# Kernel tuning notes

Measured on AMD Instinct MI355X. Metric: run time of the kernel, lower is better.

## Reference

```python
import jax, jax.numpy as jnp
import numpy as np

B, C, D, H, W = 4, 64, 16, 32, 32
K = 1024  # num_embeddings


def setup_inputs() -> dict:
    key = jax.random.key(0)
    k1, k2 = jax.random.split(key)
    z_e = jax.random.normal(k1, (B, C, D, H, W), dtype=jnp.float32)
    embedding = jax.random.normal(k2, (K, C), dtype=jnp.float32)
    return {"z_e": z_e, "embedding": embedding}


def reference(z_e, embedding):
    Bb, Cc, Dd, Hh, Ww = z_e.shape
    # (B, D, H, W, C) -> (N, C)
    flat = jnp.transpose(z_e, (0, 2, 3, 4, 1)).reshape(-1, Cc)
    # squared-euclidean distances to codebook: [N, K]
    distances = (
        jnp.sum(flat * flat, axis=1, keepdims=True)
        - 2.0 * flat @ embedding.T
        + jnp.sum(embedding * embedding, axis=1)
    )
    encoding_indices = jnp.argmin(distances, axis=1)  # [N]
    # one_hot @ embedding == gather (same math, efficient form)
    quantized_flat = embedding[encoding_indices]  # [N, C]
    quantized = jnp.transpose(
        quantized_flat.reshape(Bb, Dd, Hh, Ww, Cc), (0, 4, 1, 2, 3)
    )
    commitment_loss = jnp.mean((jax.lax.stop_gradient(quantized) - z_e) ** 2)
    codebook_loss = jnp.mean((quantized - jax.lax.stop_gradient(z_e)) ** 2)
    # straight-through estimator
    quantized_st = z_e + jax.lax.stop_gradient(quantized - z_e)
    indices = encoding_indices.reshape(Bb, Dd, Hh, Ww)
    return quantized_st, codebook_loss, commitment_loss, indices
```

## Files before the change

kernel.cpp:

```cpp
#include <hip/hip_runtime.h>

#define NPOS    65536
#define CDIM    64
#define KCODES  1024
#define SPATIAL 16384
#define QELEMS  4194304

#define PB      128
#define KT      128
#define NTILE   8

#define LOSS_IDX 1024

__device__ __forceinline__ int sig(int q)  { return (q >> 1) | ((q & 1) << 4); }
__device__ __forceinline__ int xcol(int p) { return 4 * sig(p >> 2) + (p & 3); }

__global__ void k_norms(const float* __restrict__ emb, float* __restrict__ wsf) {
    const int k = blockIdx.x * 256 + threadIdx.x;
    if (k == 0) wsf[LOSS_IDX] = 0.0f;
    const float4* e4 = (const float4*)(emb + (size_t)k * CDIM);
    float s = 0.0f;
#pragma unroll
    for (int c = 0; c < CDIM / 4; ++c) {
        float4 e = e4[c];
        s += e.x * e.x + e.y * e.y + e.z * e.z + e.w * e.w;
    }
    wsf[k] = s;
}

#define FMA_ROW(i, xs) \
    acc[i][0] = fmaf(xs, ea.x, acc[i][0]); acc[i][1] = fmaf(xs, ea.y, acc[i][1]); \
    acc[i][2] = fmaf(xs, ea.z, acc[i][2]); acc[i][3] = fmaf(xs, ea.w, acc[i][3]); \
    acc[i][4] = fmaf(xs, eb.x, acc[i][4]); acc[i][5] = fmaf(xs, eb.y, acc[i][5]); \
    acc[i][6] = fmaf(xs, eb.z, acc[i][6]); acc[i][7] = fmaf(xs, eb.w, acc[i][7]);

__global__ void k_fused(const float* __restrict__ z_e,
                        const float* __restrict__ emb,
                        float* __restrict__ out,
                        float* __restrict__ wsf) {
    __shared__ float XT[CDIM][PB];
    __shared__ float ET[CDIM][KT];
    __shared__ float NRM[KCODES];
    __shared__ unsigned long long bestp[PB];
    __shared__ int bi[PB];

    const int t    = threadIdx.x;
    const int tx   = t & 15;
    const int ty   = t >> 4;
    const int n0   = blockIdx.x * PB;
    const int b    = n0 >> 14;
    const int dhw0 = n0 & (SPATIAL - 1);
    const float* zb = z_e + (size_t)b * (CDIM * SPATIAL) + dhw0;

#pragma unroll
    for (int i = 0; i < 32; ++i) {
        const int idx = i * 256 + t;
        const int c = idx >> 7, p = idx & 127;
        XT[c][xcol(p)] = zb[(size_t)c * SPATIAL + p];
    }
    *(float4*)&NRM[4 * t] = *(const float4*)(wsf + 4 * t);

    const int crow  = t & 127;
    const int cpart = (t >> 7) << 5;
    const int ecol  = xcol(crow);
    float4 g0, g1, g2, g3, g4, g5, g6, g7;
    {
        const float* es = emb + (size_t)crow * CDIM + cpart;
        g0 = *(const float4*)(es +  0); g1 = *(const float4*)(es +  4);
        g2 = *(const float4*)(es +  8); g3 = *(const float4*)(es + 12);
        g4 = *(const float4*)(es + 16); g5 = *(const float4*)(es + 20);
        g6 = *(const float4*)(es + 24); g7 = *(const float4*)(es + 28);
    }

    unsigned long long best8[8];
#pragma unroll
    for (int i = 0; i < 8; ++i) best8[i] = ~0ull;

#pragma unroll 1
    for (int tile = 0; tile < NTILE; ++tile) {
        __syncthreads();
        ET[cpart +  0][ecol] = g0.x; ET[cpart +  1][ecol] = g0.y;
        ET[cpart +  2][ecol] = g0.z; ET[cpart +  3][ecol] = g0.w;
        ET[cpart +  4][ecol] = g1.x; ET[cpart +  5][ecol] = g1.y;
        ET[cpart +  6][ecol] = g1.z; ET[cpart +  7][ecol] = g1.w;
        ET[cpart +  8][ecol] = g2.x; ET[cpart +  9][ecol] = g2.y;
        ET[cpart + 10][ecol] = g2.z; ET[cpart + 11][ecol] = g2.w;
        ET[cpart + 12][ecol] = g3.x; ET[cpart + 13][ecol] = g3.y;
        ET[cpart + 14][ecol] = g3.z; ET[cpart + 15][ecol] = g3.w;
        ET[cpart + 16][ecol] = g4.x; ET[cpart + 17][ecol] = g4.y;
        ET[cpart + 18][ecol] = g4.z; ET[cpart + 19][ecol] = g4.w;
        ET[cpart + 20][ecol] = g5.x; ET[cpart + 21][ecol] = g5.y;
        ET[cpart + 22][ecol] = g5.z; ET[cpart + 23][ecol] = g5.w;
        ET[cpart + 24][ecol] = g6.x; ET[cpart + 25][ecol] = g6.y;
        ET[cpart + 26][ecol] = g6.z; ET[cpart + 27][ecol] = g6.w;
        ET[cpart + 28][ecol] = g7.x; ET[cpart + 29][ecol] = g7.y;
        ET[cpart + 30][ecol] = g7.z; ET[cpart + 31][ecol] = g7.w;
        if (tile + 1 < NTILE) {
            const float* es = emb + (size_t)((tile + 1) * KT + crow) * CDIM + cpart;
            g0 = *(const float4*)(es +  0); g1 = *(const float4*)(es +  4);
            g2 = *(const float4*)(es +  8); g3 = *(const float4*)(es + 12);
            g4 = *(const float4*)(es + 16); g5 = *(const float4*)(es + 20);
            g6 = *(const float4*)(es + 24); g7 = *(const float4*)(es + 28);
        }
        __syncthreads();

        float acc[8][8];
#pragma unroll
        for (int i = 0; i < 8; ++i)
#pragma unroll
            for (int j = 0; j < 8; ++j) acc[i][j] = 0.0f;

        for (int g = 0; g < 16; ++g) {
#pragma unroll
            for (int cj = 0; cj < 4; ++cj) {
                const int ch = 4 * g + cj;
                const float4 ea = *(const float4*)&ET[ch][4 * tx];
                const float4 eb = *(const float4*)&ET[ch][4 * tx + 64];
                const float4 xa = *(const float4*)&XT[ch][4 * ty];
                const float4 xb = *(const float4*)&XT[ch][4 * ty + 64];
                FMA_ROW(0, xa.x) FMA_ROW(1, xa.y) FMA_ROW(2, xa.z) FMA_ROW(3, xa.w)
                FMA_ROW(4, xb.x) FMA_ROW(5, xb.y) FMA_ROW(6, xb.z) FMA_ROW(7, xb.w)
            }
        }

        const float4 nra = *(const float4*)&NRM[tile * KT + 8 * tx];
        const float4 nrb = *(const float4*)&NRM[tile * KT + 8 * tx + 4];
        const float nv[8] = {nra.x, nra.y, nra.z, nra.w, nrb.x, nrb.y, nrb.z, nrb.w};
#pragma unroll
        for (int j = 0; j < 8; ++j) {
            const unsigned gk = (unsigned)(tile * KT + 8 * tx + j);
#pragma unroll
            for (int i = 0; i < 8; ++i) {
                const float s = fmaf(-2.0f, acc[i][j], nv[j]);
                unsigned u    = __float_as_uint(s);
                unsigned mono = (u & 0x80000000u) ? ~u : (u | 0x80000000u);
                unsigned long long pk = ((unsigned long long)mono << 10) | gk;
                if (pk < best8[i]) best8[i] = pk;
            }
        }
    }

#pragma unroll
    for (int off = 1; off < 16; off <<= 1)
#pragma unroll
        for (int i = 0; i < 8; ++i) {
            unsigned long long o = __shfl_xor(best8[i], off, 64);
            if (o < best8[i]) best8[i] = o;
        }
    if (tx == 0)
#pragma unroll
        for (int i = 0; i < 8; ++i) bestp[8 * ty + i] = best8[i];
    __syncthreads();

    if (t < PB) {
        const int bx = (int)(bestp[t] & 1023ull);
        bi[t] = bx;
        out[QELEMS + 2 + n0 + t] = (float)bx;
    }
    __syncthreads();

    float lsum = 0.0f;
    float* qb = out + (size_t)b * (CDIM * SPATIAL) + dhw0;
#pragma unroll
    for (int i = 0; i < 32; ++i) {
        const int idx = i * 256 + t;
        const int c = idx >> 7, p = idx & 127;
        const float xv = XT[c][xcol(p)];
        const float ev = emb[(size_t)bi[p] * CDIM + c];
        const float d  = ev - xv;
        qb[(size_t)c * SPATIAL + p] = xv + d;
        lsum = fmaf(d, d, lsum);
    }
#pragma unroll
    for (int off = 32; off > 0; off >>= 1) lsum += __shfl_down(lsum, off, 64);
    if ((t & 63) == 0) atomicAdd(&wsf[LOSS_IDX], lsum);
}

__global__ void k_loss(const float* __restrict__ wsf, float* __restrict__ out) {
    const float m = wsf[LOSS_IDX] / (float)QELEMS;
    out[QELEMS]     = m;
    out[QELEMS + 1] = m;
}

extern "C" void kernel_launch(void* const* d_in, const int* in_sizes, int n_in,
                              void* d_out, int out_size, void* d_ws, size_t ws_size,
                              hipStream_t stream) {
    const float* z_e = (const float*)d_in[0];
    const float* emb = (const float*)d_in[1];
    float*       out = (float*)d_out;
    float*       wsf = (float*)d_ws;

    k_norms<<<KCODES / 256, 256, 0, stream>>>(emb, wsf);
    k_fused<<<NPOS / PB, 256, 0, stream>>>(z_e, emb, out, wsf);
    k_loss<<<1, 1, 0, stream>>>(wsf, out);
}
```

Before: 258.2 us.

## Fuse norm and loss kernels into main kernel with last-block finalize

Removes the separate codebook-norm kernel and loss-finalize kernel. Each block now recomputes all 1024 codebook norms into shared memory itself, and the last block to finish, found through an atomic counter, writes the mean loss. A memset clears the accumulator and counter, and launch bounds ask for two blocks per CU. This trades two kernel launches for redundant norm work in every one of the 512 blocks (256 KB of codebook reads each, mostly served from cache) and an extra memset call.

```diff
diff --git a/kernel.cpp b/kernel.cpp
--- a/kernel.cpp
+++ b/kernel.cpp
@@ -9,24 +9,11 @@
 #define PB      128
 #define KT      128
 #define NTILE   8
-
-#define LOSS_IDX 1024
+#define NBLK    (NPOS / PB)
+
 
 __device__ __forceinline__ int sig(int q)  { return (q >> 1) | ((q & 1) << 4); }
 __device__ __forceinline__ int xcol(int p) { return 4 * sig(p >> 2) + (p & 3); }
-
-__global__ void k_norms(const float* __restrict__ emb, float* __restrict__ wsf) {
-    const int k = blockIdx.x * 256 + threadIdx.x;
-    if (k == 0) wsf[LOSS_IDX] = 0.0f;
-    const float4* e4 = (const float4*)(emb + (size_t)k * CDIM);
-    float s = 0.0f;
-#pragma unroll
-    for (int c = 0; c < CDIM / 4; ++c) {
-        float4 e = e4[c];
-        s += e.x * e.x + e.y * e.y + e.z * e.z + e.w * e.w;
-    }
-    wsf[k] = s;
-}
 
 #define FMA_ROW(i, xs) \
     acc[i][0] = fmaf(xs, ea.x, acc[i][0]); acc[i][1] = fmaf(xs, ea.y, acc[i][1]); \
@@ -34,10 +21,11 @@
     acc[i][4] = fmaf(xs, eb.x, acc[i][4]); acc[i][5] = fmaf(xs, eb.y, acc[i][5]); \
     acc[i][6] = fmaf(xs, eb.z, acc[i][6]); acc[i][7] = fmaf(xs, eb.w, acc[i][7]);
 
-__global__ void k_fused(const float* __restrict__ z_e,
-                        const float* __restrict__ emb,
-                        float* __restrict__ out,
-                        float* __restrict__ wsf) {
+__global__ __launch_bounds__(256, 2) void k_fused(const float* __restrict__ z_e,
+                                                  const float* __restrict__ emb,
+                                                  float* __restrict__ out,
+                                                  float* __restrict__ wsf,
+                                                  unsigned* __restrict__ cnt) {
     __shared__ float XT[CDIM][PB];
     __shared__ float ET[CDIM][KT];
     __shared__ float NRM[KCODES];
@@ -58,7 +46,19 @@
         const int c = idx >> 7, p = idx & 127;
         XT[c][xcol(p)] = zb[(size_t)c * SPATIAL + p];
     }
-    *(float4*)&NRM[4 * t] = *(const float4*)(wsf + 4 * t);
+
+#pragma unroll
+    for (int j = 0; j < 4; ++j) {
+        const int k = t + 256 * j;
+        const float4* e4 = (const float4*)(emb + (size_t)k * CDIM);
+        float s = 0.0f;
+#pragma unroll
+        for (int c = 0; c < CDIM / 4; ++c) {
+            float4 e = e4[c];
+            s += e.x * e.x + e.y * e.y + e.z * e.z + e.w * e.w;
+        }
+        NRM[k] = s;
+    }
 
     const int crow  = t & 127;
     const int cpart = (t >> 7) << 5;
@@ -173,13 +173,19 @@
     }
 #pragma unroll
     for (int off = 32; off > 0; off >>= 1) lsum += __shfl_down(lsum, off, 64);
-    if ((t & 63) == 0) atomicAdd(&wsf[LOSS_IDX], lsum);
-}
-
-__global__ void k_loss(const float* __restrict__ wsf, float* __restrict__ out) {
-    const float m = wsf[LOSS_IDX] / (float)QELEMS;
-    out[QELEMS]     = m;
-    out[QELEMS + 1] = m;
+    if ((t & 63) == 0) atomicAdd(&wsf[0], lsum);
+
+    __syncthreads();
+    if (t == 0) {
+        __threadfence();
+        const unsigned old = atomicAdd(cnt, 1u);
+        if (old == NBLK - 1) {
+            const float tot = atomicAdd(&wsf[0], 0.0f);
+            const float m   = tot / (float)QELEMS;
+            out[QELEMS]     = m;
+            out[QELEMS + 1] = m;
+        }
+    }
 }
 
 extern "C" void kernel_launch(void* const* d_in, const int* in_sizes, int n_in,
@@ -189,8 +195,8 @@
     const float* emb = (const float*)d_in[1];
     float*       out = (float*)d_out;
     float*       wsf = (float*)d_ws;
-
-    k_norms<<<KCODES / 256, 256, 0, stream>>>(emb, wsf);
-    k_fused<<<NPOS / PB, 256, 0, stream>>>(z_e, emb, out, wsf);
-    k_loss<<<1, 1, 0, stream>>>(wsf, out);
+    unsigned*    cnt = (unsigned*)d_ws + 1;
+
+    hipMemsetAsync(d_ws, 0, 8, stream);
+    k_fused<<<NBLK, 256, 0, stream>>>(z_e, emb, out, wsf, cnt);
 }
```

Result: faster. 210.5 us (-18.5%).
